# Kernel optimization log

Hardware: AMD Instinct MI355X
Metric: run time of the kernel (lower is better)

Reference implementation:

```python
import jax, jax.numpy as jnp
import numpy as np

N_DIMS = 16  # n points per block; nAngs = n*(n-1)/2 = 120


def orthmtx(angles, n):
    """Batched Givens-rotation cascade: angles (B, n(n-1)/2) -> (B, n, n) orthonormal."""
    nb = angles.shape[0]
    M = jnp.broadcast_to(jnp.eye(n, dtype=angles.dtype), (nb, n, n))
    k = 0
    for iTop in range(n - 1):
        vt = M[:, iTop, :]  # (B, n)
        for iBtm in range(iTop + 1, n):
            a = angles[:, k]
            c = jnp.cos(a)[:, None]
            s = jnp.sin(a)[:, None]
            vb = M[:, iBtm, :]
            vt, vb = c * vt - s * vb, s * vt + c * vb
            M = M.at[:, iBtm, :].set(vb)
            k += 1
        M = M.at[:, iTop, :].set(vt)
    return M


def setup_inputs() -> dict:
    key = jax.random.key(0)
    k1, k2 = jax.random.split(key)
    nblks, n, m = 1024, N_DIMS, 2048
    nangs = n * (n - 1) // 2
    X = jax.random.normal(k1, (nblks, n, m), dtype=jnp.float32)
    angles = jax.random.normal(k2, (nblks, nangs), dtype=jnp.float32)
    mus = jnp.ones((nblks, n), dtype=jnp.float32)
    return {"X": X, "angles": angles, "mus": mus}


def reference(X, angles, mus):
    n = X.shape[1]
    R = orthmtx(angles, n)                # (B, n, n)
    R = mus[:, :, None] * R              # sign flips per row
    return jnp.matmul(R, X)              # Analysis mode: R @ X -> (B, n, m)
```

## Files before the change

### kernel.cpp

```cpp
#include <hip/hip_runtime.h>

#define NDIM   16
#define MCOLS  2048
#define NANG   120
#define BLOCK  256
#define COLS_PER_WG 1024

typedef float f32x4 __attribute__((ext_vector_type(4)));

__global__ __launch_bounds__(BLOCK) void soot_kernel(
    const float* __restrict__ X,
    const float* __restrict__ angles,
    const float* __restrict__ mus,
    float* __restrict__ out)
{
    __shared__ float c_lds[NANG];
    __shared__ float s_lds[NANG];
    __shared__ __align__(16) float R_lds[NDIM * NDIM];

    const int wg   = blockIdx.x;
    const int b    = wg >> 1;
    const int half = wg & 1;
    const int tid  = threadIdx.x;

    if (tid < 64) {
#pragma unroll
        for (int rep = 0; rep < 2; ++rep) {
            const int k = tid + rep * 64;
            if (k < NANG) {
                float a = angles[b * NANG + k];
                float sv, cv;
                sincosf(a, &sv, &cv);
                c_lds[k] = cv;
                s_lds[k] = sv;
            }
        }
    }
    __syncthreads();

    if (tid < NDIM) {
        const int j = tid;
        float m[NDIM];
#pragma unroll
        for (int r = 0; r < NDIM; ++r) m[r] = (r == j) ? 1.0f : 0.0f;
        int k = 0;
#pragma unroll
        for (int iTop = 0; iTop < NDIM - 1; ++iTop) {
            float vt = m[iTop];
#pragma unroll
            for (int iBtm = iTop + 1; iBtm < NDIM; ++iBtm) {
                const float c  = c_lds[k];
                const float s  = s_lds[k];
                const float vb = m[iBtm];
                const float nvt = c * vt - s * vb;
                m[iBtm] = s * vt + c * vb;
                vt = nvt;
                ++k;
            }
            m[iTop] = vt;
        }
#pragma unroll
        for (int r = 0; r < NDIM; ++r)
            R_lds[r * NDIM + j] = mus[b * NDIM + r] * m[r];
    }
    __syncthreads();

    const int col = half * COLS_PER_WG + tid * 4;
    const float* Xb = X   + (size_t)b * NDIM * MCOLS;
    float*       Ob = out + (size_t)b * NDIM * MCOLS;

    f32x4 x[8];
    f32x4 acc[NDIM];

#pragma unroll
    for (int j = 0; j < 8; ++j)
        x[j] = *reinterpret_cast<const f32x4*>(Xb + j * MCOLS + col);
#pragma unroll
    for (int r = 0; r < NDIM; ++r) {
        acc[r] = R_lds[r * NDIM + 0] * x[0];
#pragma unroll
        for (int q = 1; q < 8; ++q)
            acc[r] += R_lds[r * NDIM + q] * x[q];
    }

#pragma unroll
    for (int j = 0; j < 8; ++j)
        x[j] = *reinterpret_cast<const f32x4*>(Xb + (8 + j) * MCOLS + col);
#pragma unroll
    for (int r = 0; r < NDIM; ++r) {
#pragma unroll
        for (int q = 0; q < 8; ++q)
            acc[r] += R_lds[r * NDIM + 8 + q] * x[q];
    }

#pragma unroll
    for (int r = 0; r < NDIM; ++r)
        __builtin_nontemporal_store(acc[r], reinterpret_cast<f32x4*>(Ob + r * MCOLS + col));
}

extern "C" void kernel_launch(void* const* d_in, const int* in_sizes, int n_in,
                              void* d_out, int out_size, void* d_ws, size_t ws_size,
                              hipStream_t stream) {
    const float* X      = (const float*)d_in[0];
    const float* angles = (const float*)d_in[1];
    const float* mus    = (const float*)d_in[2];
    float* out          = (float*)d_out;

    const int nblks = in_sizes[1] / NANG;
    dim3 grid(nblks * (MCOLS / COLS_PER_WG));
    dim3 block(BLOCK);
    hipLaunchKernelGGL(soot_kernel, grid, block, 0, stream,
                       X, angles, mus, out);
}
```

Before: 46.23 us.

## Process both column halves per workgroup with software-pipelined loads

Each workgroup now handles a whole block of 2048 columns instead of half, so the angle sincos and Givens-cascade R construction happen once per block rather than twice. Loads for both row halves are issued up front, and loads for the second column half are interleaved with compute and stores of the first half to overlap memory latency. This halves the grid to 1024 workgroups and raises register pressure (x0, x1, acc live together), which may lower occupancy.

New measurement: 57.50 us. +24.4%, slower.

```diff
diff --git a/kernel.cpp b/kernel.cpp
--- a/kernel.cpp
+++ b/kernel.cpp
@@ -4,7 +4,7 @@
 #define MCOLS  2048
 #define NANG   120
 #define BLOCK  256
-#define COLS_PER_WG 1024
+#define HALFC  1024
 
 typedef float f32x4 __attribute__((ext_vector_type(4)));
 
@@ -18,10 +18,8 @@
     __shared__ float s_lds[NANG];
     __shared__ __align__(16) float R_lds[NDIM * NDIM];
 
-    const int wg   = blockIdx.x;
-    const int b    = wg >> 1;
-    const int half = wg & 1;
-    const int tid  = threadIdx.x;
+    const int b   = blockIdx.x;
+    const int tid = threadIdx.x;
 
     if (tid < 64) {
 #pragma unroll
@@ -65,37 +63,61 @@
     }
     __syncthreads();
 
-    const int col = half * COLS_PER_WG + tid * 4;
     const float* Xb = X   + (size_t)b * NDIM * MCOLS;
     float*       Ob = out + (size_t)b * NDIM * MCOLS;
+    const int c0 = tid * 4;
+    const int c1 = HALFC + tid * 4;
 
-    f32x4 x[8];
-    f32x4 acc[NDIM];
+    f32x4 x0[8], x1[8], acc[NDIM];
 
 #pragma unroll
     for (int j = 0; j < 8; ++j)
-        x[j] = *reinterpret_cast<const f32x4*>(Xb + j * MCOLS + col);
+        x0[j] = *reinterpret_cast<const f32x4*>(Xb + j * MCOLS + c0);
+#pragma unroll
+    for (int j = 0; j < 8; ++j)
+        x1[j] = *reinterpret_cast<const f32x4*>(Xb + (8 + j) * MCOLS + c0);
+
 #pragma unroll
     for (int r = 0; r < NDIM; ++r) {
-        acc[r] = R_lds[r * NDIM + 0] * x[0];
+        acc[r] = R_lds[r * NDIM + 0] * x0[0];
 #pragma unroll
         for (int q = 1; q < 8; ++q)
-            acc[r] += R_lds[r * NDIM + q] * x[q];
+            acc[r] += R_lds[r * NDIM + q] * x0[q];
     }
-
 #pragma unroll
     for (int j = 0; j < 8; ++j)
-        x[j] = *reinterpret_cast<const f32x4*>(Xb + (8 + j) * MCOLS + col);
+        x0[j] = *reinterpret_cast<const f32x4*>(Xb + j * MCOLS + c1);
+
 #pragma unroll
     for (int r = 0; r < NDIM; ++r) {
 #pragma unroll
         for (int q = 0; q < 8; ++q)
-            acc[r] += R_lds[r * NDIM + 8 + q] * x[q];
+            acc[r] += R_lds[r * NDIM + 8 + q] * x1[q];
     }
+#pragma unroll
+    for (int j = 0; j < 8; ++j)
+        x1[j] = *reinterpret_cast<const f32x4*>(Xb + (8 + j) * MCOLS + c1);
 
 #pragma unroll
     for (int r = 0; r < NDIM; ++r)
-        __builtin_nontemporal_store(acc[r], reinterpret_cast<f32x4*>(Ob + r * MCOLS + col));
+        __builtin_nontemporal_store(acc[r], reinterpret_cast<f32x4*>(Ob + r * MCOLS + c0));
+
+#pragma unroll
+    for (int r = 0; r < NDIM; ++r) {
+        acc[r] = R_lds[r * NDIM + 0] * x0[0];
+#pragma unroll
+        for (int q = 1; q < 8; ++q)
+            acc[r] += R_lds[r * NDIM + q] * x0[q];
+    }
+#pragma unroll
+    for (int r = 0; r < NDIM; ++r) {
+#pragma unroll
+        for (int q = 0; q < 8; ++q)
+            acc[r] += R_lds[r * NDIM + 8 + q] * x1[q];
+    }
+#pragma unroll
+    for (int r = 0; r < NDIM; ++r)
+        __builtin_nontemporal_store(acc[r], reinterpret_cast<f32x4*>(Ob + r * MCOLS + c1));
 }
 
 extern "C" void kernel_launch(void* const* d_in, const int* in_sizes, int n_in,
@@ -107,8 +129,6 @@
     float* out          = (float*)d_out;
 
     const int nblks = in_sizes[1] / NANG;
-    dim3 grid(nblks * (MCOLS / COLS_PER_WG));
-    dim3 block(BLOCK);
-    hipLaunchKernelGGL(soot_kernel, grid, block, 0, stream,
+    hipLaunchKernelGGL(soot_kernel, dim3(nblks), dim3(BLOCK), 0, stream,
                        X, angles, mus, out);
 }
```
